# Optimization experiments

Hardware: AMD Instinct MI355X
Metric: run time of the kernel (lower is better)

The kernel has to match this reference:

```python
import jax, jax.numpy as jnp
import numpy as np

G, A = 1024, 20          # graphs, atoms per graph
N = G * A                # nodes = 20480
E = G * A * A            # fc edges within each graph = 409600
H = 128                  # hidden_dim
LATENT = 256             # latent_dim
L = 4                    # num_layers
NFREQ = 10
DIS_DIM = NFREQ * 2 * 3  # 60
EDGE_IN = 2 * H + 9 + DIS_DIM  # 325
MAX_ATOMS = 100


def _lin(k, fin, fout):
    return jax.random.normal(k, (fin, fout), dtype=jnp.float32) / np.sqrt(fin).astype(np.float32)


def _stack_lin(k, fin, fout):
    return jnp.stack([_lin(jax.random.fold_in(k, i), fin, fout) for i in range(L)])


def setup_inputs() -> dict:
    key = jax.random.key(0)
    ks = jax.random.split(key, 16)
    atom_types = jax.random.randint(ks[0], (N,), 0, MAX_ATOMS, dtype=jnp.int32)
    frac_coords = jax.random.uniform(ks[1], (N, 3), dtype=jnp.float32)
    lattices = jax.random.normal(ks[2], (G, 3, 3), dtype=jnp.float32)
    t = jax.random.normal(ks[3], (G, LATENT), dtype=jnp.float32)
    # fully-connected (fc) edges within each graph, block-diagonal structure
    base = np.arange(A)
    src = np.repeat(base, A)
    dst = np.tile(base, A)
    offs = (np.arange(G) * A)[:, None]
    edge_index = jnp.asarray(np.stack([
        (src[None, :] + offs).reshape(-1),
        (dst[None, :] + offs).reshape(-1)]), dtype=jnp.int32)  # [2, E]
    edge2graph = jnp.asarray(np.repeat(np.arange(G), A * A), dtype=jnp.int32)
    node2graph = jnp.asarray(np.repeat(np.arange(G), A), dtype=jnp.int32)
    # parameters
    emb_table = jax.random.normal(ks[4], (MAX_ATOMS, H), dtype=jnp.float32) * 0.02
    w_latent = _lin(ks[5], H + LATENT, H)
    b_latent = jnp.zeros((H,), jnp.float32)
    edge_w1 = _stack_lin(ks[6], EDGE_IN, H)
    edge_b1 = jnp.zeros((L, H), jnp.float32)
    edge_w2 = _stack_lin(ks[7], H, H)
    edge_b2 = jnp.zeros((L, H), jnp.float32)
    node_w1 = _stack_lin(ks[8], 2 * H, H)
    node_b1 = jnp.zeros((L, H), jnp.float32)
    node_w2 = _stack_lin(ks[9], H, H)
    node_b2 = jnp.zeros((L, H), jnp.float32)
    coord_w = _lin(ks[10], H, 3)
    lattice_w = _lin(ks[11], H, 9)
    return dict(atom_types=atom_types, frac_coords=frac_coords, lattices=lattices, t=t,
                edge_index=edge_index, edge2graph=edge2graph, node2graph=node2graph,
                emb_table=emb_table, w_latent=w_latent, b_latent=b_latent,
                edge_w1=edge_w1, edge_b1=edge_b1, edge_w2=edge_w2, edge_b2=edge_b2,
                node_w1=node_w1, node_b1=node_b1, node_w2=node_w2, node_b2=node_b2,
                coord_w=coord_w, lattice_w=lattice_w)


def reference(atom_types, frac_coords, lattices, t, edge_index, edge2graph, node2graph,
              emb_table, w_latent, b_latent,
              edge_w1, edge_b1, edge_w2, edge_b2,
              node_w1, node_b1, node_w2, node_b2,
              coord_w, lattice_w):
    silu = jax.nn.silu
    src, dst = edge_index[0], edge_index[1]
    # node embedding + latent conditioning
    h = emb_table[atom_types]                               # [N,H]
    h = jnp.concatenate([h, t[node2graph]], axis=1) @ w_latent + b_latent  # [N,H]
    # sinusoidal distance embedding of periodic frac diff (detached in original)
    frac_diff = (frac_coords[dst] - frac_coords[src]) % 1.0  # [E,3]
    freqs = 2.0 * jnp.pi * jnp.arange(NFREQ, dtype=frac_coords.dtype)
    emb = (frac_diff[..., None] * freqs).reshape(-1, 3 * NFREQ)
    dis = jax.lax.stop_gradient(jnp.concatenate([jnp.sin(emb), jnp.cos(emb)], axis=-1))  # [E,60]
    # lattice inner products, broadcast to edges (ip=True)
    lat_ip = jnp.einsum('gij,gkj->gik', lattices, lattices).reshape(-1, 9)
    lat_edges = lat_ip[edge2graph]                          # [E,9]
    # per-node edge counts for scatter-mean
    counts = jax.ops.segment_sum(jnp.ones_like(src, dtype=h.dtype), src, num_segments=N)
    inv_counts = (1.0 / jnp.maximum(counts, 1.0))[:, None]
    for i in range(L):
        e_in = jnp.concatenate([h[src], h[dst], lat_edges, dis], axis=1)  # [E,325]
        ef = silu(e_in @ edge_w1[i] + edge_b1[i])
        ef = silu(ef @ edge_w2[i] + edge_b2[i])               # [E,H]
        agg = jax.ops.segment_sum(ef, src, num_segments=N) * inv_counts   # scatter-mean
        n_in = jnp.concatenate([h, agg], axis=1)              # [N,2H]
        nf = silu(n_in @ node_w1[i] + node_b1[i])
        nf = silu(nf @ node_w2[i] + node_b2[i])
        h = h + nf                                            # residual
    coord_out = h @ coord_w                                   # [N,3]
    gcounts = jax.ops.segment_sum(jnp.ones((h.shape[0],), h.dtype), node2graph, num_segments=G)
    graph_feat = jax.ops.segment_sum(h, node2graph, num_segments=G) / gcounts[:, None]
    lattice_out = (graph_feat @ lattice_w).reshape(-1, 3, 3)
    lattice_out = jnp.einsum('bij,bjk->bik', lattice_out, lattices)  # ip=True
    return lattice_out, coord_out
```

## Files before the change

kernel.cpp:

```cpp
#include <hip/hip_runtime.h>
#include <stdint.h>


#define NA 20
#define HH 128

typedef unsigned short U16;
typedef unsigned int   U32;
typedef __attribute__((ext_vector_type(8))) short bf8;
typedef __attribute__((ext_vector_type(4))) float f4;

__device__ __forceinline__ float bf2f(U16 u){ return __uint_as_float(((U32)u)<<16); }
__device__ __forceinline__ U16 f2bf(float f){
    return (U16)((__float_as_uint(f) + 0x8000u) >> 16);
}
__device__ __forceinline__ float silu_f(float x){ return x/(1.0f+__expf(-x)); }
template<bool BF>
__device__ __forceinline__ float ldf(const void* p, long i){
    return BF ? bf2f(((const U16*)p)[i]) : ((const float*)p)[i];
}
__device__ __forceinline__ f4 mfma(bf8 a, bf8 b, f4 c){
    return __builtin_amdgcn_mfma_f32_16x16x32_bf16(a,b,c,0,0,0);
}
__device__ __forceinline__ bf8 ldsA(const U16* base, int stride, int row0,
                                    int kbase, int lrow, int quad){
    return *(const bf8*)(base + (row0+lrow)*stride + kbase + quad*8);
}
template<bool BF, bool WS>
__device__ __forceinline__ bf8 getB(const U16* wsb, long wbase, int kt, int nt,
                                    int lane, const void* W, long gbase, int N,
                                    int col, int kbase, int kmax, int quad){
    if constexpr(WS){
        return *(const bf8*)(wsb + wbase + (((long)kt*8 + nt)*64 + lane)*8);
    } else {
        bf8 b; int ks0 = kbase + quad*8;
#pragma unroll
        for(int j=0;j<8;j++){
            int k=ks0+j; U16 v=0;
            if(k<kmax) v = BF ? ((const U16*)W)[gbase+(long)k*N+col]
                              : f2bf(((const float*)W)[gbase+(long)k*N+col]);
            b[j]=(short)v;
        }
        return b;
    }
}

#define WS_LBASE(L) (49152 + (long)(L)*106496)
#define REPACK_BYTES 950272

__global__ __launch_bounds__(256) void repack(
    const void* wlat, const void* ew1, const void* ew2,
    const void* nw1p, const void* nw2p, const void* lat, U16* out)
{
    __shared__ int sG[4];
    const int tid=threadIdx.x;
    {
        const U16* l16=(const U16*)lat; int good=0;
#pragma unroll
        for(int u=0;u<32;u++){
            U16 x=l16[tid*32+u]; int e=(x>>7)&0xFF; good+=(e>=100&&e<=150)?1:0;
        }
#pragma unroll
        for(int o=32;o>0;o>>=1) good+=__shfl_xor(good,o);
        if((tid&63)==0) sG[tid>>6]=good;
    }
    __syncthreads();
    const bool bf = (sG[0]+sG[1]+sG[2]+sG[3]) > 6144;

    const void* W; long srow; int segk; long dst;
    const int ktg=blockIdx.x;
    if(ktg<12){ W=wlat; srow=(long)ktg*32; segk=32; dst=(long)ktg*4096; }
    else{
        int r=ktg-12, L=r/26, lk=r-26*L;
        dst = 49152 + (long)L*106496 + (long)lk*4096;
        if(lk<4)      { W=ew1;  srow=(long)L*325+lk*32;          segk=32; }
        else if(lk<8) { W=ew1;  srow=(long)L*325+128+(lk-4)*32;  segk=32; }
        else if(lk<10){ W=ew1;  srow=(long)L*325+265+(lk-8)*32;  segk=60-(lk-8)*32; }
        else if(lk<14){ W=ew2;  srow=(long)L*128+(lk-10)*32;     segk=32; }
        else if(lk<22){ W=nw1p; srow=(long)L*256+(lk-14)*32;     segk=32; }
        else          { W=nw2p; srow=(long)L*128+(lk-22)*32;     segk=32; }
    }
    for(int o=tid;o<4096;o+=256){
        int nt=o>>9, lane=(o>>3)&63, j=o&7;
        int kk=((lane>>4)<<3)+j, col=nt*16+(lane&15);
        U16 v=0;
        if(kk<segk){
            long idx=(srow+kk)*128+col;
            v = bf ? ((const U16*)W)[idx] : f2bf(((const float*)W)[idx]);
        }
        out[dst+o]=v;
    }
}

#define PB_OFF 8960
#define QB_OFF 11520
#define DB_OFF 14080
#define EB_OFF 19840

template<bool BF, bool WS>
__device__ void body(U16* sm, float* red, const U16* wsb, int g, int tid,
    const int* __restrict__ atype, const void* frac, const void* lattices,
    const void* t, const void* emb, const void* wlat, const void* blat,
    const void* ew1, const void* eb1, const void* ew2, const void* eb2,
    const void* nw1p, const void* nb1, const void* nw2p, const void* nb2,
    const void* coordw, const void* latw, void* outv)
{
    const int lane=tid&63, w=tid>>6, lrow=lane&15, quad=lane>>4;
    const int c = w*16 + lrow;
    U16* HA=sm; U16* pB=sm+PB_OFF; U16* qB=sm+QB_OFF;
    U16* dB=sm+DB_OFF; U16* eB=sm+EB_OFF;
    U16* k1A=eB;
    float* tvecF=(float*)dB;

    for(int q=tid;q<8960;q+=512) HA[q]=0;
    for(int q=tid;q<32*136;q+=512){
        int n=q/136, cc=q-n*136; U16 v=0;
        if(n<20 && cc<128)
            v = BF ? ((const U16*)emb)[(long)atype[g*NA+n]*HH+cc]
                   : f2bf(((const float*)emb)[(long)atype[g*NA+n]*HH+cc]);
        k1A[q]=v;
    }
    {
        int sl=tid>>7, j=tid&127; float acc=0.f;
        for(int kk=0;kk<64;kk++){
            int k=sl*64+kk;
            acc += ldf<BF>(t,(long)g*256+k)*ldf<BF>(wlat,(long)(HH+k)*HH+j);
        }
        tvecF[sl*128+j]=acc;
    }
    __syncthreads();
    {
        f4 a0={0.f,0.f,0.f,0.f}, a1={0.f,0.f,0.f,0.f};
#pragma unroll
        for(int ks=0;ks<4;ks++){
            bf8 b=getB<BF,WS>(wsb,0,ks,w,lane, wlat,0,HH,c,ks*32,128,quad);
            bf8 v0=ldsA(k1A,136,0,ks*32,lrow,quad);
            bf8 v1=ldsA(k1A,136,16,ks*32,lrow,quad);
            a0=mfma(v0,b,a0); a1=mfma(v1,b,a1);
        }
        float bias=ldf<BF>(blat,c)+tvecF[c]+tvecF[128+c]+tvecF[256+c]+tvecF[384+c];
#pragma unroll
        for(int r=0;r<4;r++){
            int r0=quad*4+r, r1=16+quad*4+r;
            if(r0<20) HA[r0*280+c]=f2bf(a0[r]+bias);
            if(r1<20) HA[r1*280+c]=f2bf(a1[r]+bias);
        }
    }
    __syncthreads();
    for(int q=tid;q<80*72;q+=512) dB[q]=0;

    for(int L=0;L<4;L++){
        const long e1=(long)L*325*HH;
        const long LB=WS_LBASE(L);
        if(tid<HH){
            float la[9];
#pragma unroll
            for(int m2=0;m2<9;m2++) la[m2]=ldf<BF>(lattices,(long)g*9+m2);
            float Rv=ldf<BF>(eb1,(long)L*HH+tid);
#pragma unroll
            for(int a2=0;a2<3;a2++)
#pragma unroll
            for(int b3=0;b3<3;b3++){
                float ip=0.f;
#pragma unroll
                for(int c2=0;c2<3;c2++) ip+=la[a2*3+c2]*la[b3*3+c2];
                Rv += ip*ldf<BF>(ew1, e1+(long)(256+a2*3+b3)*HH+tid);
            }
            red[tid]=Rv;
        }
        __syncthreads();
        {
            f4 p0={0.f,0.f,0.f,0.f}, p1={0.f,0.f,0.f,0.f};
#pragma unroll
            for(int ks=0;ks<4;ks++){
                bf8 b=getB<BF,WS>(wsb,LB,ks,w,lane, ew1,e1,HH,c,ks*32,128,quad);
                bf8 v0=ldsA(HA,280,0,ks*32,lrow,quad);
                bf8 v1=ldsA(HA,280,16,ks*32,lrow,quad);
                p0=mfma(v0,b,p0); p1=mfma(v1,b,p1);
            }
            float Rc=red[c];
#pragma unroll
            for(int r=0;r<4;r++){
                int r0=quad*4+r, r1=16+quad*4+r;
                if(r0<20) pB[r0*HH+c]=f2bf(p0[r]+Rc);
                if(r1<20) pB[r1*HH+c]=f2bf(p1[r]+Rc);
            }
        }
        {
            f4 q0={0.f,0.f,0.f,0.f}, q1={0.f,0.f,0.f,0.f};
#pragma unroll
            for(int ks=0;ks<4;ks++){
                bf8 b=getB<BF,WS>(wsb,LB+16384,ks,w,lane, ew1,e1+128*HH,HH,c,ks*32,128,quad);
                bf8 v0=ldsA(HA,280,0,ks*32,lrow,quad);
                bf8 v1=ldsA(HA,280,16,ks*32,lrow,quad);
                q0=mfma(v0,b,q0); q1=mfma(v1,b,q1);
            }
#pragma unroll
            for(int r=0;r<4;r++){
                int r0=quad*4+r, r1=16+quad*4+r;
                if(r0<20) qB[r0*HH+c]=f2bf(q0[r]);
                if(r1<20) qB[r1*HH+c]=f2bf(q1[r]);
            }
        }
        bf8 w1d0=getB<BF,WS>(wsb,LB+32768,0,w,lane, ew1,e1+(long)265*HH,HH,c,0, 60,quad);
        bf8 w1d1=getB<BF,WS>(wsb,LB+32768,1,w,lane, ew1,e1+(long)265*HH,HH,c,32,60,quad);
        bf8 w2f[4];
#pragma unroll
        for(int ks=0;ks<4;ks++)
            w2f[ks]=getB<BF,WS>(wsb,LB+40960,ks,w,lane, ew2,(long)L*HH*HH,HH,c,ks*32,128,quad);
        const float b2=ldf<BF>(eb2,(long)L*HH+c);
        __syncthreads();

        for(int ch=0;ch<5;ch++){
            for(int p=tid;p<2400;p+=512){
                int r=p/30, kk=p-r*30;
                int dim=kk/10, f=kk-dim*10;
                int s=ch*4+(r&3), d=r>>2;
                float fs=ldf<BF>(frac,(long)(g*NA+s)*3+dim);
                float fd=ldf<BF>(frac,(long)(g*NA+d)*3+dim);
                float rev=(float)f*(fd-fs);
                rev=__builtin_amdgcn_fractf(rev);
                dB[r*72+kk]   =f2bf(__builtin_amdgcn_sinf(rev));
                dB[r*72+kk+30]=f2bf(__builtin_amdgcn_cosf(rev));
            }
            __syncthreads();
            float pv[4];
#pragma unroll
            for(int r=0;r<4;r++) pv[r]=bf2f(pB[(ch*4+r)*HH+c]);
#pragma unroll
            for(int m=0;m<5;m++){
                f4 a={0.f,0.f,0.f,0.f};
                bf8 v0=ldsA(dB,72,m*16,0, lrow,quad);
                bf8 v1=ldsA(dB,72,m*16,32,lrow,quad);
                a=mfma(v0,w1d0,a); a=mfma(v1,w1d1,a);
                float qd=bf2f(qB[(m*4+quad)*HH+c]);
#pragma unroll
                for(int r=0;r<4;r++){
                    int row=m*16+quad*4+r;
                    eB[row*136+c]=f2bf(silu_f(a[r]+pv[r]+qd));
                }
            }
            __syncthreads();
            float part[4]={0.f,0.f,0.f,0.f};
#pragma unroll
            for(int m=0;m<5;m++){
                f4 a={0.f,0.f,0.f,0.f};
#pragma unroll
                for(int ks=0;ks<4;ks++){
                    bf8 v=ldsA(eB,136,m*16,ks*32,lrow,quad);
                    a=mfma(v,w2f[ks],a);
                }
#pragma unroll
                for(int r=0;r<4;r++) part[r]+=silu_f(a[r]+b2);
            }
#pragma unroll
            for(int r=0;r<4;r++){
                float v=part[r];
                v+=__shfl_xor(v,16); v+=__shfl_xor(v,32);
                part[r]=v;
            }
            if(quad==0){
#pragma unroll
                for(int r=0;r<4;r++)
                    HA[(ch*4+r)*280+128+c]=f2bf(part[r]*0.05f);
            }
            __syncthreads();
        }
        {
            f4 a0={0.f,0.f,0.f,0.f}, a1={0.f,0.f,0.f,0.f};
#pragma unroll
            for(int ks=0;ks<8;ks++){
                bf8 b=getB<BF,WS>(wsb,LB+57344,ks,w,lane, nw1p,(long)L*256*HH,HH,c,ks*32,256,quad);
                bf8 v0=ldsA(HA,280,0,ks*32,lrow,quad);
                bf8 v1=ldsA(HA,280,16,ks*32,lrow,quad);
                a0=mfma(v0,b,a0); a1=mfma(v1,b,a1);
            }
            float n1=ldf<BF>(nb1,(long)L*HH+c);
#pragma unroll
            for(int r=0;r<4;r++){
                int r0=quad*4+r, r1=16+quad*4+r;
                eB[r0*136+c]=f2bf(r0<20 ? silu_f(a0[r]+n1) : 0.f);
                eB[r1*136+c]=f2bf(r1<20 ? silu_f(a1[r]+n1) : 0.f);
            }
        }
        __syncthreads();
        {
            f4 a0={0.f,0.f,0.f,0.f}, a1={0.f,0.f,0.f,0.f};
#pragma unroll
            for(int ks=0;ks<4;ks++){
                bf8 b=getB<BF,WS>(wsb,LB+90112,ks,w,lane, nw2p,(long)L*HH*HH,HH,c,ks*32,128,quad);
                bf8 v0=ldsA(eB,136,0,ks*32,lrow,quad);
                bf8 v1=ldsA(eB,136,16,ks*32,lrow,quad);
                a0=mfma(v0,b,a0); a1=mfma(v1,b,a1);
            }
            float n2=ldf<BF>(nb2,(long)L*HH+c);
#pragma unroll
            for(int r=0;r<4;r++){
                int r0=quad*4+r, r1=16+quad*4+r;
                if(r0<20) HA[r0*280+c]=f2bf(bf2f(HA[r0*280+c])+silu_f(a0[r]+n2));
                if(r1<20) HA[r1*280+c]=f2bf(bf2f(HA[r1*280+c])+silu_f(a1[r]+n2));
            }
        }
        __syncthreads();
    }

    if(tid<60){
        int n=tid/3, cc=tid-(tid/3)*3; float acc=0.f;
        for(int k=0;k<HH;k++) acc+=bf2f(HA[n*280+k])*ldf<BF>(coordw,(long)k*3+cc);
        if(BF) ((U16*)outv)[(long)1024*9+(long)(g*NA+n)*3+cc]=f2bf(acc);
        else   ((float*)outv)[(long)1024*9+(long)(g*NA+n)*3+cc]=acc;
    }
    if(tid<HH){
        float s2=0.f;
        for(int n=0;n<NA;n++) s2+=bf2f(HA[n*280+tid]);
        red[tid]=s2*0.05f;
    }
    __syncthreads();
    if(tid<9){
        float acc=0.f;
        for(int k=0;k<HH;k++) acc+=red[k]*ldf<BF>(latw,(long)k*9+tid);
        red[HH+tid]=acc;
    }
    __syncthreads();
    if(tid<9){
        int i2=tid/3, k2=tid-(tid/3)*3; float acc=0.f;
#pragma unroll
        for(int j3=0;j3<3;j3++)
            acc+=red[HH+i2*3+j3]*ldf<BF>(lattices,(long)g*9+j3*3+k2);
        if(BF) ((U16*)outv)[(long)g*9+tid]=f2bf(acc);
        else   ((float*)outv)[(long)g*9+tid]=acc;
    }
}

template<bool WS>
__device__ void mega_impl(const U16* wsb,
    const int* atype, const void* frac, const void* lattices, const void* t,
    const void* emb, const void* wlat, const void* blat,
    const void* ew1, const void* eb1, const void* ew2, const void* eb2,
    const void* nw1p, const void* nb1, const void* nw2p, const void* nb2,
    const void* coordw, const void* latw, void* outv)
{
    __shared__ __align__(16) unsigned char smraw[62080];
    U16* sm = (U16*)smraw;
    float* red = (float*)(smraw+61440);
    const int g=blockIdx.x, tid=threadIdx.x, w=tid>>6, lane=tid&63;
    int* di=(int*)red;
    {
        const U16* l16=(const U16*)lattices; int good=0;
#pragma unroll
        for(int u=0;u<16;u++){
            U16 x=l16[tid*16+u]; int e=(x>>7)&0xFF; good+=(e>=100&&e<=150)?1:0;
        }
#pragma unroll
        for(int o=32;o>0;o>>=1) good+=__shfl_xor(good,o);
        if(lane==0) di[w]=good;
    }
    __syncthreads();
    if(tid==0){ int s=0; for(int i=0;i<8;i++) s+=di[i]; di[8]=(s>6144)?1:0; }
    __syncthreads();
    const int bfm=di[8];
    __syncthreads();
    if(bfm) body<true ,WS>(sm,red,wsb,g,tid,atype,frac,lattices,t,emb,wlat,blat,
                           ew1,eb1,ew2,eb2,nw1p,nb1,nw2p,nb2,coordw,latw,outv);
    else    body<false,WS>(sm,red,wsb,g,tid,atype,frac,lattices,t,emb,wlat,blat,
                           ew1,eb1,ew2,eb2,nw1p,nb1,nw2p,nb2,coordw,latw,outv);
}

__global__ __launch_bounds__(512,2) void mega_ws(const U16* wsb,
    const int* atype, const void* frac, const void* lattices, const void* t,
    const void* emb, const void* wlat, const void* blat,
    const void* ew1, const void* eb1, const void* ew2, const void* eb2,
    const void* nw1p, const void* nb1, const void* nw2p, const void* nb2,
    const void* coordw, const void* latw, void* outv)
{
    mega_impl<true>(wsb,atype,frac,lattices,t,emb,wlat,blat,ew1,eb1,ew2,eb2,
                    nw1p,nb1,nw2p,nb2,coordw,latw,outv);
}

__global__ __launch_bounds__(512,2) void mega_direct(const U16* wsb,
    const int* atype, const void* frac, const void* lattices, const void* t,
    const void* emb, const void* wlat, const void* blat,
    const void* ew1, const void* eb1, const void* ew2, const void* eb2,
    const void* nw1p, const void* nb1, const void* nw2p, const void* nb2,
    const void* coordw, const void* latw, void* outv)
{
    mega_impl<false>(wsb,atype,frac,lattices,t,emb,wlat,blat,ew1,eb1,ew2,eb2,
                     nw1p,nb1,nw2p,nb2,coordw,latw,outv);
}

extern "C" void kernel_launch(void* const* d_in, const int* in_sizes, int n_in,
                              void* d_out, int out_size, void* d_ws, size_t ws_size,
                              hipStream_t stream)
{
    (void)in_sizes; (void)n_in; (void)out_size;
    const int* atype = (const int*)d_in[0];
    if(ws_size >= REPACK_BYTES){
        repack<<<116, 256, 0, stream>>>(d_in[8], d_in[10], d_in[12], d_in[14],
                                        d_in[16], d_in[2], (U16*)d_ws);
        mega_ws<<<1024, 512, 0, stream>>>((const U16*)d_ws,
            atype, d_in[1], d_in[2], d_in[3], d_in[7], d_in[8], d_in[9],
            d_in[10], d_in[11], d_in[12], d_in[13], d_in[14], d_in[15],
            d_in[16], d_in[17], d_in[18], d_in[19], d_out);
    } else {
        mega_direct<<<1024, 512, 0, stream>>>(nullptr,
            atype, d_in[1], d_in[2], d_in[3], d_in[7], d_in[8], d_in[9],
            d_in[10], d_in[11], d_in[12], d_in[13], d_in[14], d_in[15],
            d_in[16], d_in[17], d_in[18], d_in[19], d_out);
    }
}
```

Measured before the change: 436.5 us.

## Keep edge projections in registers, cache frac in LDS, shrink LDS footprint

```diff
diff --git a/kernel.cpp b/kernel.cpp
--- a/kernel.cpp
+++ b/kernel.cpp
@@ -92,13 +92,12 @@
     }
 }
 
-#define PB_OFF 8960
-#define QB_OFF 11520
-#define DB_OFF 14080
-#define EB_OFF 19840
+#define DB_OFF 8448
+#define EB_OFF 14208
 
 template<bool BF, bool WS>
-__device__ void body(U16* sm, float* red, const U16* wsb, int g, int tid,
+__device__ void body(U16* sm, float* red4, float* fracS, const U16* wsb,
+    int g, int tid,
     const int* __restrict__ atype, const void* frac, const void* lattices,
     const void* t, const void* emb, const void* wlat, const void* blat,
     const void* ew1, const void* eb1, const void* ew2, const void* eb2,
@@ -107,27 +106,24 @@
 {
     const int lane=tid&63, w=tid>>6, lrow=lane&15, quad=lane>>4;
     const int c = w*16 + lrow;
-    U16* HA=sm; U16* pB=sm+PB_OFF; U16* qB=sm+QB_OFF;
-    U16* dB=sm+DB_OFF; U16* eB=sm+EB_OFF;
+    U16* HA=sm; U16* dB=sm+DB_OFF; U16* eB=sm+EB_OFF;
     U16* k1A=eB;
-    float* tvecF=(float*)dB;
-
-    for(int q=tid;q<8960;q+=512) HA[q]=0;
-    for(int q=tid;q<32*136;q+=512){
-        int n=q/136, cc=q-n*136; U16 v=0;
-        if(n<20 && cc<128)
-            v = BF ? ((const U16*)emb)[(long)atype[g*NA+n]*HH+cc]
-                   : f2bf(((const float*)emb)[(long)atype[g*NA+n]*HH+cc]);
-        k1A[q]=v;
-    }
-    {
-        int sl=tid>>7, j=tid&127; float acc=0.f;
+    float* tvecF=(float*)(eB+4096);
+
+    if(tid<60) fracS[tid]=ldf<BF>(frac,(long)g*60+tid);
+    for(int q=tid;q<20*128;q+=512){
+        int n=q>>7, cc=q&127;
+        k1A[n*136+cc] = BF ? ((const U16*)emb)[(long)atype[g*NA+n]*HH+cc]
+                           : f2bf(((const float*)emb)[(long)atype[g*NA+n]*HH+cc]);
+    }
+    {   int sl=tid>>7, j=tid&127; float acc=0.f;
         for(int kk=0;kk<64;kk++){
             int k=sl*64+kk;
             acc += ldf<BF>(t,(long)g*256+k)*ldf<BF>(wlat,(long)(HH+k)*HH+j);
         }
         tvecF[sl*128+j]=acc;
     }
+    for(int q=tid;q<80*72;q+=512) dB[q]=0;
     __syncthreads();
     {
         f4 a0={0.f,0.f,0.f,0.f}, a1={0.f,0.f,0.f,0.f};
@@ -142,65 +138,45 @@
 #pragma unroll
         for(int r=0;r<4;r++){
             int r0=quad*4+r, r1=16+quad*4+r;
-            if(r0<20) HA[r0*280+c]=f2bf(a0[r]+bias);
-            if(r1<20) HA[r1*280+c]=f2bf(a1[r]+bias);
-        }
-    }
-    __syncthreads();
-    for(int q=tid;q<80*72;q+=512) dB[q]=0;
+            if(r0<20) HA[r0*264+c]=f2bf(a0[r]+bias);
+            if(r1<20) HA[r1*264+c]=f2bf(a1[r]+bias);
+        }
+    }
+    {
+        int L=tid>>7, j=tid&127;
+        float la[9];
+#pragma unroll
+        for(int m2=0;m2<9;m2++) la[m2]=ldf<BF>(lattices,(long)g*9+m2);
+        float Rv=ldf<BF>(eb1,(long)L*HH+j);
+#pragma unroll
+        for(int a2=0;a2<3;a2++)
+#pragma unroll
+        for(int b3=0;b3<3;b3++){
+            float ip=0.f;
+#pragma unroll
+            for(int c2=0;c2<3;c2++) ip+=la[a2*3+c2]*la[b3*3+c2];
+            Rv += ip*ldf<BF>(ew1,(long)(L*325+256+a2*3+b3)*HH+j);
+        }
+        red4[L*128+j]=Rv;
+    }
+    __syncthreads();
 
     for(int L=0;L<4;L++){
         const long e1=(long)L*325*HH;
         const long LB=WS_LBASE(L);
-        if(tid<HH){
-            float la[9];
-#pragma unroll
-            for(int m2=0;m2<9;m2++) la[m2]=ldf<BF>(lattices,(long)g*9+m2);
-            float Rv=ldf<BF>(eb1,(long)L*HH+tid);
-#pragma unroll
-            for(int a2=0;a2<3;a2++)
-#pragma unroll
-            for(int b3=0;b3<3;b3++){
-                float ip=0.f;
-#pragma unroll
-                for(int c2=0;c2<3;c2++) ip+=la[a2*3+c2]*la[b3*3+c2];
-                Rv += ip*ldf<BF>(ew1, e1+(long)(256+a2*3+b3)*HH+tid);
-            }
-            red[tid]=Rv;
-        }
-        __syncthreads();
-        {
-            f4 p0={0.f,0.f,0.f,0.f}, p1={0.f,0.f,0.f,0.f};
-#pragma unroll
-            for(int ks=0;ks<4;ks++){
-                bf8 b=getB<BF,WS>(wsb,LB,ks,w,lane, ew1,e1,HH,c,ks*32,128,quad);
-                bf8 v0=ldsA(HA,280,0,ks*32,lrow,quad);
-                bf8 v1=ldsA(HA,280,16,ks*32,lrow,quad);
-                p0=mfma(v0,b,p0); p1=mfma(v1,b,p1);
-            }
-            float Rc=red[c];
-#pragma unroll
-            for(int r=0;r<4;r++){
-                int r0=quad*4+r, r1=16+quad*4+r;
-                if(r0<20) pB[r0*HH+c]=f2bf(p0[r]+Rc);
-                if(r1<20) pB[r1*HH+c]=f2bf(p1[r]+Rc);
-            }
-        }
-        {
-            f4 q0={0.f,0.f,0.f,0.f}, q1={0.f,0.f,0.f,0.f};
-#pragma unroll
-            for(int ks=0;ks<4;ks++){
-                bf8 b=getB<BF,WS>(wsb,LB+16384,ks,w,lane, ew1,e1+128*HH,HH,c,ks*32,128,quad);
-                bf8 v0=ldsA(HA,280,0,ks*32,lrow,quad);
-                bf8 v1=ldsA(HA,280,16,ks*32,lrow,quad);
-                q0=mfma(v0,b,q0); q1=mfma(v1,b,q1);
-            }
-#pragma unroll
-            for(int r=0;r<4;r++){
-                int r0=quad*4+r, r1=16+quad*4+r;
-                if(r0<20) qB[r0*HH+c]=f2bf(q0[r]);
-                if(r1<20) qB[r1*HH+c]=f2bf(q1[r]);
-            }
+        f4 p0={0.f,0.f,0.f,0.f}, p1=p0, q0=p0, q1=p0;
+#pragma unroll
+        for(int ks=0;ks<4;ks++){
+            bf8 bp=getB<BF,WS>(wsb,LB,      ks,w,lane, ew1,e1,       HH,c,ks*32,128,quad);
+            bf8 bq=getB<BF,WS>(wsb,LB+16384,ks,w,lane, ew1,e1+128*HH,HH,c,ks*32,128,quad);
+            bf8 v0=ldsA(HA,264,0,ks*32,lrow,quad);
+            bf8 v1=ldsA(HA,264,16,ks*32,lrow,quad);
+            p0=mfma(v0,bp,p0); p1=mfma(v1,bp,p1);
+            q0=mfma(v0,bq,q0); q1=mfma(v1,bq,q1);
+        }
+        {   float Rc=red4[L*128+c];
+#pragma unroll
+            for(int r=0;r<4;r++){ p0[r]+=Rc; p1[r]+=Rc; }
         }
         bf8 w1d0=getB<BF,WS>(wsb,LB+32768,0,w,lane, ew1,e1+(long)265*HH,HH,c,0, 60,quad);
         bf8 w1d1=getB<BF,WS>(wsb,LB+32768,1,w,lane, ew1,e1+(long)265*HH,HH,c,32,60,quad);
@@ -209,35 +185,46 @@
         for(int ks=0;ks<4;ks++)
             w2f[ks]=getB<BF,WS>(wsb,LB+40960,ks,w,lane, ew2,(long)L*HH*HH,HH,c,ks*32,128,quad);
         const float b2=ldf<BF>(eb2,(long)L*HH+c);
+        for(int p=tid;p<2400;p+=512){
+            int r=p/30, kk=p-r*30;
+            int dim=kk/10, f=kk-dim*10;
+            int s=r&3, d=r>>2;
+            float x=fracS[d*3+dim]-fracS[s*3+dim];
+            float rev=__builtin_amdgcn_fractf((float)f*x);
+            dB[r*72+kk]   =f2bf(__builtin_amdgcn_sinf(rev));
+            dB[r*72+kk+30]=f2bf(__builtin_amdgcn_cosf(rev));
+        }
         __syncthreads();
 
         for(int ch=0;ch<5;ch++){
-            for(int p=tid;p<2400;p+=512){
-                int r=p/30, kk=p-r*30;
-                int dim=kk/10, f=kk-dim*10;
-                int s=ch*4+(r&3), d=r>>2;
-                float fs=ldf<BF>(frac,(long)(g*NA+s)*3+dim);
-                float fd=ldf<BF>(frac,(long)(g*NA+d)*3+dim);
-                float rev=(float)f*(fd-fs);
-                rev=__builtin_amdgcn_fractf(rev);
-                dB[r*72+kk]   =f2bf(__builtin_amdgcn_sinf(rev));
-                dB[r*72+kk+30]=f2bf(__builtin_amdgcn_cosf(rev));
-            }
-            __syncthreads();
             float pv[4];
-#pragma unroll
-            for(int r=0;r<4;r++) pv[r]=bf2f(pB[(ch*4+r)*HH+c]);
+            if(ch<4){
+#pragma unroll
+                for(int r=0;r<4;r++) pv[r]=__shfl(p0[r],(ch<<4)|lrow);
+            } else {
+#pragma unroll
+                for(int r=0;r<4;r++) pv[r]=__shfl(p1[r],lrow);
+            }
 #pragma unroll
             for(int m=0;m<5;m++){
                 f4 a={0.f,0.f,0.f,0.f};
                 bf8 v0=ldsA(dB,72,m*16,0, lrow,quad);
                 bf8 v1=ldsA(dB,72,m*16,32,lrow,quad);
                 a=mfma(v0,w1d0,a); a=mfma(v1,w1d1,a);
-                float qd=bf2f(qB[(m*4+quad)*HH+c]);
+                float t0,t1,t2,t3;
+                if(m<4){
+                    int sl=(m<<4)|lrow;
+                    t0=__shfl(q0[0],sl); t1=__shfl(q0[1],sl);
+                    t2=__shfl(q0[2],sl); t3=__shfl(q0[3],sl);
+                } else {
+                    t0=__shfl(q1[0],lrow); t1=__shfl(q1[1],lrow);
+                    t2=__shfl(q1[2],lrow); t3=__shfl(q1[3],lrow);
+                }
+                float qv = quad==0?t0: quad==1?t1: quad==2?t2:t3;
 #pragma unroll
                 for(int r=0;r<4;r++){
                     int row=m*16+quad*4+r;
-                    eB[row*136+c]=f2bf(silu_f(a[r]+pv[r]+qd));
+                    eB[row*136+c]=f2bf(silu_f(a[r]+pv[r]+qv));
                 }
             }
             __syncthreads();
@@ -262,7 +249,18 @@
             if(quad==0){
 #pragma unroll
                 for(int r=0;r<4;r++)
-                    HA[(ch*4+r)*280+128+c]=f2bf(part[r]*0.05f);
+                    HA[(ch*4+r)*264+128+c]=f2bf(part[r]*0.05f);
+            }
+            if(ch<4){
+                for(int p=tid;p<2400;p+=512){
+                    int r=p/30, kk=p-r*30;
+                    int dim=kk/10, f=kk-dim*10;
+                    int s=(ch+1)*4+(r&3), d=r>>2;
+                    float x=fracS[d*3+dim]-fracS[s*3+dim];
+                    float rev=__builtin_amdgcn_fractf((float)f*x);
+                    dB[r*72+kk]   =f2bf(__builtin_amdgcn_sinf(rev));
+                    dB[r*72+kk+30]=f2bf(__builtin_amdgcn_cosf(rev));
+                }
             }
             __syncthreads();
         }
@@ -271,16 +269,16 @@
 #pragma unroll
             for(int ks=0;ks<8;ks++){
                 bf8 b=getB<BF,WS>(wsb,LB+57344,ks,w,lane, nw1p,(long)L*256*HH,HH,c,ks*32,256,quad);
-                bf8 v0=ldsA(HA,280,0,ks*32,lrow,quad);
-                bf8 v1=ldsA(HA,280,16,ks*32,lrow,quad);
+                bf8 v0=ldsA(HA,264,0,ks*32,lrow,quad);
+                bf8 v1=ldsA(HA,264,16,ks*32,lrow,quad);
                 a0=mfma(v0,b,a0); a1=mfma(v1,b,a1);
             }
             float n1=ldf<BF>(nb1,(long)L*HH+c);
 #pragma unroll
             for(int r=0;r<4;r++){
                 int r0=quad*4+r, r1=16+quad*4+r;
-                eB[r0*136+c]=f2bf(r0<20 ? silu_f(a0[r]+n1) : 0.f);
-                eB[r1*136+c]=f2bf(r1<20 ? silu_f(a1[r]+n1) : 0.f);
+                eB[r0*136+c]=f2bf(silu_f(a0[r]+n1));
+                if(r1<20) eB[r1*136+c]=f2bf(silu_f(a1[r]+n1));
             }
         }
         __syncthreads();
@@ -297,36 +295,61 @@
 #pragma unroll
             for(int r=0;r<4;r++){
                 int r0=quad*4+r, r1=16+quad*4+r;
-                if(r0<20) HA[r0*280+c]=f2bf(bf2f(HA[r0*280+c])+silu_f(a0[r]+n2));
-                if(r1<20) HA[r1*280+c]=f2bf(bf2f(HA[r1*280+c])+silu_f(a1[r]+n2));
+                if(r0<20) HA[r0*264+c]=f2bf(bf2f(HA[r0*264+c])+silu_f(a0[r]+n2));
+                if(r1<20) HA[r1*264+c]=f2bf(bf2f(HA[r1*264+c])+silu_f(a1[r]+n2));
             }
         }
         __syncthreads();
     }
 
+    float* meanF=(float*)dB;
+    if(tid<480){
+        int n=tid/24, rem=tid-(tid/24)*24, cc=rem>>3, kg=rem&7;
+        float acc=0.f;
+#pragma unroll
+        for(int u=0;u<16;u++){
+            int k=kg*16+u;
+            acc+=bf2f(HA[n*264+k])*ldf<BF>(coordw,(long)k*3+cc);
+        }
+        red4[tid]=acc;
+    }
+    if(tid<HH){
+        float s2=0.f;
+        for(int n=0;n<NA;n++) s2+=bf2f(HA[n*264+tid]);
+        meanF[tid]=s2*0.05f;
+    }
+    __syncthreads();
     if(tid<60){
-        int n=tid/3, cc=tid-(tid/3)*3; float acc=0.f;
-        for(int k=0;k<HH;k++) acc+=bf2f(HA[n*280+k])*ldf<BF>(coordw,(long)k*3+cc);
+        int n=tid/3, cc=tid-(tid/3)*3;
+        float acc=0.f;
+#pragma unroll
+        for(int kg=0;kg<8;kg++) acc+=red4[n*24+cc*8+kg];
         if(BF) ((U16*)outv)[(long)1024*9+(long)(g*NA+n)*3+cc]=f2bf(acc);
         else   ((float*)outv)[(long)1024*9+(long)(g*NA+n)*3+cc]=acc;
     }
-    if(tid<HH){
-        float s2=0.f;
-        for(int n=0;n<NA;n++) s2+=bf2f(HA[n*280+tid]);
-        red[tid]=s2*0.05f;
+    if(tid>=64 && tid<136){
+        int u=tid-64, i=u>>3, kg=u&7;
+        float acc=0.f;
+#pragma unroll
+        for(int v=0;v<16;v++){
+            int k=kg*16+v;
+            acc+=meanF[k]*ldf<BF>(latw,(long)k*9+i);
+        }
+        red4[512+u]=acc;
     }
     __syncthreads();
     if(tid<9){
         float acc=0.f;
-        for(int k=0;k<HH;k++) acc+=red[k]*ldf<BF>(latw,(long)k*9+tid);
-        red[HH+tid]=acc;
+#pragma unroll
+        for(int kg=0;kg<8;kg++) acc+=red4[512+tid*8+kg];
+        red4[600+tid]=acc;
     }
     __syncthreads();
     if(tid<9){
         int i2=tid/3, k2=tid-(tid/3)*3; float acc=0.f;
 #pragma unroll
         for(int j3=0;j3<3;j3++)
-            acc+=red[HH+i2*3+j3]*ldf<BF>(lattices,(long)g*9+j3*3+k2);
+            acc+=red4[600+i2*3+j3]*ldf<BF>(lattices,(long)g*9+j3*3+k2);
         if(BF) ((U16*)outv)[(long)g*9+tid]=f2bf(acc);
         else   ((float*)outv)[(long)g*9+tid]=acc;
     }
@@ -340,11 +363,12 @@
     const void* nw1p, const void* nb1, const void* nw2p, const void* nb2,
     const void* coordw, const void* latw, void* outv)
 {
-    __shared__ __align__(16) unsigned char smraw[62080];
+    __shared__ __align__(16) unsigned char smraw[52976];
     U16* sm = (U16*)smraw;
-    float* red = (float*)(smraw+61440);
+    float* red4 = (float*)(smraw+50176);
+    float* fracS = (float*)(smraw+52736);
     const int g=blockIdx.x, tid=threadIdx.x, w=tid>>6, lane=tid&63;
-    int* di=(int*)red;
+    int* di=(int*)red4;
     {
         const U16* l16=(const U16*)lattices; int good=0;
 #pragma unroll
@@ -360,13 +384,13 @@
     __syncthreads();
     const int bfm=di[8];
     __syncthreads();
-    if(bfm) body<true ,WS>(sm,red,wsb,g,tid,atype,frac,lattices,t,emb,wlat,blat,
+    if(bfm) body<true ,WS>(sm,red4,fracS,wsb,g,tid,atype,frac,lattices,t,emb,wlat,blat,
                            ew1,eb1,ew2,eb2,nw1p,nb1,nw2p,nb2,coordw,latw,outv);
-    else    body<false,WS>(sm,red,wsb,g,tid,atype,frac,lattices,t,emb,wlat,blat,
+    else    body<false,WS>(sm,red4,fracS,wsb,g,tid,atype,frac,lattices,t,emb,wlat,blat,
                            ew1,eb1,ew2,eb2,nw1p,nb1,nw2p,nb2,coordw,latw,outv);
 }
 
-__global__ __launch_bounds__(512,2) void mega_ws(const U16* wsb,
+__global__ __launch_bounds__(512,6) void mega_ws(const U16* wsb,
     const int* atype, const void* frac, const void* lattices, const void* t,
     const void* emb, const void* wlat, const void* blat,
     const void* ew1, const void* eb1, const void* ew2, const void* eb2,
@@ -377,7 +401,7 @@
                     nw1p,nb1,nw2p,nb2,coordw,latw,outv);
 }
 
-__global__ __launch_bounds__(512,2) void mega_direct(const U16* wsb,
+__global__ __launch_bounds__(512,6) void mega_direct(const U16* wsb,
     const int* atype, const void* frac, const void* lattices, const void* t,
     const void* emb, const void* wlat, const void* blat,
     const void* ew1, const void* eb1, const void* ew2, const void* eb2,
```

New measurement: 507.5 us. 1.16x slower.
